# Performance work log

Measured on AMD Instinct MI355X. Metric: run time of the kernel, lower is better.

The kernel has to match this reference:

```python
import jax, jax.numpy as jnp
import numpy as np

LORA_DIM = 16          # hard-coded in module
LORA_TOKEN_INDEX = 1   # lora_dim*layer_sequence + 1 with layer_sequence=0
B, S, D, H = 4, 2048, 1024, 4096  # num_hiddens = 4*num_input (forced by view())


def setup_inputs() -> dict:
    key = jax.random.key(0)
    ks = jax.random.split(key, 6)
    x = jax.random.normal(ks[0], (B, S, D), dtype=jnp.float32)
    W1 = jax.random.normal(ks[1], (H, D), dtype=jnp.float32) * 0.02
    b1 = jnp.zeros((H,), dtype=jnp.float32)
    W2 = jax.random.normal(ks[2], (D, H), dtype=jnp.float32) * 0.02
    b2 = jnp.zeros((D,), dtype=jnp.float32)
    scale = jnp.asarray(0.001, dtype=jnp.float32)  # nn.Parameter(torch.tensor(0.001))
    return {"x": x, "W1": W1, "b1": b1, "W2": W2, "b2": b2, "scale": scale}


def reference(x, W1, b1, W2, b2, scale):
    Bx, Sx, Dx = x.shape
    Hx = W1.shape[0]  # = 4*Dx
    # 16 lora tokens starting at LORA_TOKEN_INDEX
    lt = jax.lax.dynamic_slice_in_dim(x, LORA_TOKEN_INDEX, LORA_DIM, axis=1)
    even = lt[:, ::2, :]  # (B, 8, D)
    odd = lt[:, 1::2, :]  # (B, 8, D)
    # per-sample low-rank weight updates:
    # result_multiplication[b,k] = outer(even[b,k], odd[b,k]) (D,D)
    # matrix1 = first 4 blocks stacked -> (B, 4D, D); matrix2 = last 4 reshaped -> (B, D, 4D)
    m1 = (even[:, :4, :, None] * odd[:, :4, None, :]).reshape(Bx, Hx, Dx)
    m2 = (even[:, 4:, :, None] * odd[:, 4:, None, :]).reshape(Bx, Dx, Hx)
    # x @ (W1 + scale*m1)^T + b1, fused without repeating W1 per batch
    h = jnp.einsum('bsd,hd->bsh', x, W1) + scale * jnp.einsum('bsd,bhd->bsh', x, m1) + b1
    h = jax.nn.gelu(h, approximate=False)  # torch nn.GELU default = exact erf
    out = jnp.einsum('bsh,oh->bso', h, W2) + scale * jnp.einsum('bsh,boh->bso', h, m2) + b2
    return out
```

## Files before the change

kernel.cpp:

```cpp
#include <hip/hip_runtime.h>
#include <cstdint>
#include <cstddef>

#define MROWS 8192
#define DDIM  1024
#define HDIM  4096

typedef __bf16 bf16x8 __attribute__((ext_vector_type(8)));
typedef float  f32x4  __attribute__((ext_vector_type(4)));

typedef __attribute__((address_space(1))) void* as1_vp;
typedef __attribute__((address_space(3))) void* as3_vp;

__device__ __forceinline__ unsigned short f2bf(float f) {
  unsigned int u = __builtin_bit_cast(unsigned int, f);
  u += 0x7fffu + ((u >> 16) & 1u);
  return (unsigned short)(u >> 16);
}
__device__ __forceinline__ float bf2f(unsigned short h) {
  return __builtin_bit_cast(float, (unsigned int)h << 16);
}

__device__ __forceinline__ float fast_gelu(float x) {
  float x3 = x * x * x;
  float z = 0.7978845608028654f * x + 0.03567740814f * x3;
  float e = __builtin_amdgcn_exp2f(z * 2.8853900817779268f);
  float t = 1.0f - 2.0f * __builtin_amdgcn_rcpf(e + 1.0f);
  return 0.5f * x * (1.0f + t);
}

__device__ __forceinline__ void gld_lds16(const unsigned short* g, unsigned short* lds) {
  __builtin_amdgcn_global_load_lds((as1_vp)(uintptr_t)g, (as3_vp)lds, 16, 0, 0);
}

__global__ __launch_bounds__(256) void pre_kernel(
    const float* __restrict__ x, const float* __restrict__ w1,
    const float* __restrict__ w2, unsigned short* __restrict__ xb,
    unsigned short* __restrict__ w1b, unsigned short* __restrict__ w2b,
    float* __restrict__ p1) {
  if (blockIdx.x < 8192) {
    int i = blockIdx.x * 256 + threadIdx.x;
    const float* src; unsigned short* dst; int off;
    if (i < 1048576) { src = w1; dst = w1b; off = i; }
    else             { src = w2; dst = w2b; off = i - 1048576; }
    float4 v = ((const float4*)src)[off];
    ushort4 o;
    o.x = f2bf(v.x); o.y = f2bf(v.y); o.z = f2bf(v.z); o.w = f2bf(v.w);
    ((ushort4*)dst)[off] = o;
    return;
  }
  const int bid = blockIdx.x - 8192;
  const int wave = threadIdx.x >> 6, lane = threadIdx.x & 63;
  const int m = bid * 4 + wave;
  const int b = m >> 11;
  const float4* xrow4 = (const float4*)(x + (size_t)m * DDIM);
  const float4* od4   = (const float4*)(x + ((size_t)b * 2048 + 2) * DDIM);
  ushort4* xbrow4 = (ushort4*)(xb + (size_t)m * DDIM);
  float a0 = 0.f, a1 = 0.f, a2 = 0.f, a3 = 0.f;
#pragma unroll
  for (int it = 0; it < 4; ++it) {
    int g = it * 64 + lane;
    float4 v = xrow4[g];
    ushort4 o; o.x = f2bf(v.x); o.y = f2bf(v.y); o.z = f2bf(v.z); o.w = f2bf(v.w);
    xbrow4[g] = o;
    float4 o0 = od4[g];
    float4 o1 = od4[512 + g];
    float4 o2 = od4[1024 + g];
    float4 o3 = od4[1536 + g];
    a0 += v.x * o0.x + v.y * o0.y + v.z * o0.z + v.w * o0.w;
    a1 += v.x * o1.x + v.y * o1.y + v.z * o1.z + v.w * o1.w;
    a2 += v.x * o2.x + v.y * o2.y + v.z * o2.z + v.w * o2.w;
    a3 += v.x * o3.x + v.y * o3.y + v.z * o3.z + v.w * o3.w;
  }
#pragma unroll
  for (int off = 32; off > 0; off >>= 1) {
    a0 += __shfl_down(a0, off);
    a1 += __shfl_down(a1, off);
    a2 += __shfl_down(a2, off);
    a3 += __shfl_down(a3, off);
  }
  if (lane == 0) {
    float4 r; r.x = a0; r.y = a1; r.z = a2; r.w = a3;
    ((float4*)p1)[m] = r;
  }
}

__global__ __launch_bounds__(256) void p2_kernel(const unsigned short* __restrict__ hact,
                                                 const float* __restrict__ x,
                                                 float* __restrict__ p2) {
  const int wave = threadIdx.x >> 6, lane = threadIdx.x & 63;
  const int m = blockIdx.x * 4 + wave;
  const int b = m >> 11;
  const ushort4* hrow4 = (const ushort4*)(hact + (size_t)m * HDIM);
  const float4* od4    = (const float4*)(x + ((size_t)b * 2048 + 10) * DDIM);
  float acc[4][4] = {{0.f}};
#pragma unroll
  for (int it = 0; it < 4; ++it) {
    int g = it * 64 + lane;
    float h[4][4];
#pragma unroll
    for (int r = 0; r < 4; ++r) {
      ushort4 hv = hrow4[r * 256 + g];
      h[r][0] = bf2f(hv.x); h[r][1] = bf2f(hv.y); h[r][2] = bf2f(hv.z); h[r][3] = bf2f(hv.w);
    }
#pragma unroll
    for (int i = 0; i < 4; ++i) {
      float4 ov = od4[i * 512 + g];
#pragma unroll
      for (int r = 0; r < 4; ++r)
        acc[i][r] += ov.x * h[r][0] + ov.y * h[r][1] + ov.z * h[r][2] + ov.w * h[r][3];
    }
  }
#pragma unroll
  for (int i = 0; i < 4; ++i)
#pragma unroll
    for (int r = 0; r < 4; ++r)
#pragma unroll
      for (int off = 32; off > 0; off >>= 1)
        acc[i][r] += __shfl_down(acc[i][r], off);
  if (lane == 0) {
#pragma unroll
    for (int i = 0; i < 4; ++i) {
      float4 v; v.x = acc[i][0]; v.y = acc[i][1]; v.z = acc[i][2]; v.w = acc[i][3];
      ((float4*)(p2 + (size_t)m * 16))[i] = v;
    }
  }
}

__device__ __forceinline__ void gemm_bt_tile64(const unsigned short* __restrict__ A,
                                               const unsigned short* __restrict__ B,
                                               const int ld, const int Kloop,
                                               const int m0, const int n0,
                                               unsigned short* As, unsigned short* Bs,
                                               f32x4 acc[4][4]) {
  const int tid  = threadIdx.x;
  const int wave = tid >> 6;
  const int lane = tid & 63;
  const int quad = lane >> 4;
  const int l16  = lane & 15;
  const int wm   = (wave >> 1) * 64;
  const int wn   = (wave & 1) * 64;

  const unsigned short* ga[4]; const unsigned short* gb[4];
#pragma unroll
  for (int s = 0; s < 4; ++s) {
    int idx = wave * 256 + s * 64 + lane;
    int r = idx >> 3, sl = idx & 7;
    int c = (sl - r) & 7;
    ga[s] = A + (size_t)(m0 + r) * ld + c * 8;
    gb[s] = B + (size_t)(n0 + r) * ld + c * 8;
  }

  for (int k0 = 0; k0 < Kloop; k0 += 64) {
    __syncthreads();
#pragma unroll
    for (int s = 0; s < 4; ++s) gld_lds16(ga[s] + k0, As + (wave * 4 + s) * 512);
#pragma unroll
    for (int s = 0; s < 4; ++s) gld_lds16(gb[s] + k0, Bs + (wave * 4 + s) * 512);
    __syncthreads();
#pragma unroll
    for (int kk = 0; kk < 64; kk += 32) {
      bf16x8 a[4], b[4];
      const int cbase = (kk >> 3) + quad;
#pragma unroll
      for (int i = 0; i < 4; ++i) {
        const int ra = wm + i * 16 + l16;
        const int rb = wn + i * 16 + l16;
        a[i] = *(const bf16x8*)(As + ra * 64 + ((cbase + ra) & 7) * 8);
        b[i] = *(const bf16x8*)(Bs + rb * 64 + ((cbase + rb) & 7) * 8);
      }
#pragma unroll
      for (int i = 0; i < 4; ++i)
#pragma unroll
        for (int j = 0; j < 4; ++j)
          acc[i][j] = __builtin_amdgcn_mfma_f32_16x16x32_bf16(a[i], b[j], acc[i][j], 0, 0, 0);
    }
  }
}

__global__ __launch_bounds__(256) void gemm1_kernel(
    const unsigned short* __restrict__ xb, const unsigned short* __restrict__ w1b,
    const float* __restrict__ x, const float* __restrict__ b1,
    const float* __restrict__ p1, const float* __restrict__ scale_p,
    unsigned short* __restrict__ hact) {
  __shared__ __align__(16) unsigned short As[128 * 64];
  __shared__ __align__(16) unsigned short Bs[128 * 64];
  const int id = blockIdx.x;
  const int xcd = id & 7, w = id >> 3;
  const int m0 = (xcd * 8 + (w & 7)) * 128;
  const int n0 = (w >> 3) * 128;
  f32x4 acc[4][4];
  const f32x4 z = {0.f, 0.f, 0.f, 0.f};
#pragma unroll
  for (int i = 0; i < 4; ++i)
#pragma unroll
    for (int j = 0; j < 4; ++j) acc[i][j] = z;

  gemm_bt_tile64(xb, w1b, DDIM, DDIM, m0, n0, As, Bs, acc);

  const int tid = threadIdx.x;
  const int wave = tid >> 6, lane = tid & 63, quad = lane >> 4, l16 = lane & 15;
  const int wm = (wave >> 1) * 64, wn = (wave & 1) * 64;
  const float sc = scale_p[0];
  const int bidx = m0 >> 11;
  const int i1 = (n0 + wn) >> 10;
  const float* exrow = x + ((size_t)(bidx * 2048 + 1 + 2 * i1)) * DDIM;

  float exv[4], b1v[4]; int nn[4];
#pragma unroll
  for (int j = 0; j < 4; ++j) {
    nn[j]  = n0 + wn + j * 16 + l16;
    exv[j] = exrow[nn[j] & 1023];
    b1v[j] = b1[nn[j]];
  }
#pragma unroll
  for (int i = 0; i < 4; ++i) {
#pragma unroll
    for (int r = 0; r < 4; ++r) {
      const int m = m0 + wm + i * 16 + quad * 4 + r;
      const float pv = p1[(size_t)m * 4 + i1] * sc;
#pragma unroll
      for (int j = 0; j < 4; ++j) {
        float v = acc[i][j][r] + b1v[j] + pv * exv[j];
        hact[(size_t)m * HDIM + nn[j]] = f2bf(fast_gelu(v));
      }
    }
  }
}

__global__ __launch_bounds__(256) void gemm2_kernel(
    const unsigned short* __restrict__ hact, const unsigned short* __restrict__ w2b,
    const float* __restrict__ x, const float* __restrict__ b2,
    const float* __restrict__ p2, const float* __restrict__ scale_p,
    float* __restrict__ out) {
  __shared__ __align__(16) unsigned short As[128 * 128];
  __shared__ __align__(16) unsigned short Bs[128 * 128];
  const int id = blockIdx.x;
  const int xcd = id & 7, w = id >> 3;
  const int m0 = (xcd * 8 + (w >> 3)) * 128;
  const int n0 = (w & 7) * 128;
  const int tid = threadIdx.x;
  const int wave = tid >> 6, lane = tid & 63, quad = lane >> 4, l16 = lane & 15;
  const int wm = (wave >> 1) * 64, wn = (wave & 1) * 64;
  f32x4 acc[4][4];
  const f32x4 z = {0.f, 0.f, 0.f, 0.f};
#pragma unroll
  for (int i = 0; i < 4; ++i)
#pragma unroll
    for (int j = 0; j < 4; ++j) acc[i][j] = z;

  const unsigned short* ga[8]; const unsigned short* gb[8];
#pragma unroll
  for (int s = 0; s < 8; ++s) {
    int idx = wave * 512 + s * 64 + lane;
    int r = idx >> 4, sl = idx & 15;
    int c = (sl - r) & 15;
    ga[s] = hact + (size_t)(m0 + r) * HDIM + c * 8;
    gb[s] = w2b  + (size_t)(n0 + r) * HDIM + c * 8;
  }

  for (int k0 = 0; k0 < HDIM; k0 += 128) {
    __syncthreads();
#pragma unroll
    for (int s = 0; s < 8; ++s) gld_lds16(ga[s] + k0, As + (wave * 8 + s) * 512);
#pragma unroll
    for (int s = 0; s < 8; ++s) gld_lds16(gb[s] + k0, Bs + (wave * 8 + s) * 512);
    __syncthreads();
#pragma unroll
    for (int kk = 0; kk < 128; kk += 32) {
      bf16x8 a[4], b[4];
      const int cbase = (kk >> 3) + quad;
#pragma unroll
      for (int i = 0; i < 4; ++i) {
        const int ra = wm + i * 16 + l16;
        const int rb = wn + i * 16 + l16;
        a[i] = *(const bf16x8*)(As + ra * 128 + ((cbase + ra) & 15) * 8);
        b[i] = *(const bf16x8*)(Bs + rb * 128 + ((cbase + rb) & 15) * 8);
      }
#pragma unroll
      for (int i = 0; i < 4; ++i)
#pragma unroll
        for (int j = 0; j < 4; ++j)
          acc[i][j] = __builtin_amdgcn_mfma_f32_16x16x32_bf16(a[i], b[j], acc[i][j], 0, 0, 0);
    }
  }

  const float sc = scale_p[0];
  const int bidx = m0 >> 11;
  const int i2 = (n0 + wn) >> 8;
  const float* evrow = x + ((size_t)(bidx * 2048 + 9 + 2 * i2)) * DDIM;

  float4 ev[4]; float b2v[4]; int nn[4];
#pragma unroll
  for (int j = 0; j < 4; ++j) {
    nn[j] = n0 + wn + j * 16 + l16;
    ev[j]  = *(const float4*)(evrow + 4 * (nn[j] & 255));
    b2v[j] = b2[nn[j]];
  }
#pragma unroll
  for (int i = 0; i < 4; ++i) {
#pragma unroll
    for (int r = 0; r < 4; ++r) {
      const int m = m0 + wm + i * 16 + quad * 4 + r;
      const float4 pv = *(const float4*)(p2 + (size_t)m * 16 + i2 * 4);
#pragma unroll
      for (int j = 0; j < 4; ++j) {
        float lora = ev[j].x * pv.x + ev[j].y * pv.y + ev[j].z * pv.z + ev[j].w * pv.w;
        out[(size_t)m * DDIM + nn[j]] = acc[i][j][r] + b2v[j] + sc * lora;
      }
    }
  }
}

extern "C" void kernel_launch(void* const* d_in, const int* in_sizes, int n_in,
                              void* d_out, int out_size, void* d_ws, size_t ws_size,
                              hipStream_t stream) {
  const float* x     = (const float*)d_in[0];
  const float* W1    = (const float*)d_in[1];
  const float* b1    = (const float*)d_in[2];
  const float* W2    = (const float*)d_in[3];
  const float* b2    = (const float*)d_in[4];
  const float* scale = (const float*)d_in[5];
  float* out = (float*)d_out;

  char* ws = (char*)d_ws;
  unsigned short* xb   = (unsigned short*)(ws);
  unsigned short* w1b  = (unsigned short*)(ws + 16777216);
  unsigned short* w2b  = (unsigned short*)(ws + 25165824);
  unsigned short* hact = (unsigned short*)(ws + 33554432);
  float*          p1   = (float*)(ws + 100663296);
  float*          p2   = (float*)(ws + 100794368);

  pre_kernel<<<dim3(10240), dim3(256), 0, stream>>>(x, W1, W2, xb, w1b, w2b, p1);
  gemm1_kernel<<<dim3(2048), dim3(256), 0, stream>>>(xb, w1b, x, b1, p1, scale, hact);
  p2_kernel<<<dim3(2048), dim3(256), 0, stream>>>(hact, x, p2);
  gemm2_kernel<<<dim3(512), dim3(256), 0, stream>>>(hact, w2b, x, b2, p2, scale, out);
}
```

Measured before the change: 282.9 us.

## Fuse p2 LoRA projection into gemm2 via extra MFMA on staged tiles

Removes the separate p2_kernel, which reread the whole bf16 hidden activation to project it onto the odd LoRA vectors. gemm2 now computes that projection inside its K loop: half the waves issue an extra MFMA per step against an odd-vector fragment kept in LDS (only lane column 0 nonzero), and write per-1024-segment partial sums to shared memory for the epilogue. This saves one full pass over hact and a kernel launch. In exchange it adds MFMA work and an imbalance between waves in gemm2, rounds the odd vector to bf16, and adds a little LDS.

```diff
diff --git a/kernel.cpp b/kernel.cpp
--- a/kernel.cpp
+++ b/kernel.cpp
@@ -85,48 +85,6 @@
   }
 }
 
-__global__ __launch_bounds__(256) void p2_kernel(const unsigned short* __restrict__ hact,
-                                                 const float* __restrict__ x,
-                                                 float* __restrict__ p2) {
-  const int wave = threadIdx.x >> 6, lane = threadIdx.x & 63;
-  const int m = blockIdx.x * 4 + wave;
-  const int b = m >> 11;
-  const ushort4* hrow4 = (const ushort4*)(hact + (size_t)m * HDIM);
-  const float4* od4    = (const float4*)(x + ((size_t)b * 2048 + 10) * DDIM);
-  float acc[4][4] = {{0.f}};
-#pragma unroll
-  for (int it = 0; it < 4; ++it) {
-    int g = it * 64 + lane;
-    float h[4][4];
-#pragma unroll
-    for (int r = 0; r < 4; ++r) {
-      ushort4 hv = hrow4[r * 256 + g];
-      h[r][0] = bf2f(hv.x); h[r][1] = bf2f(hv.y); h[r][2] = bf2f(hv.z); h[r][3] = bf2f(hv.w);
-    }
-#pragma unroll
-    for (int i = 0; i < 4; ++i) {
-      float4 ov = od4[i * 512 + g];
-#pragma unroll
-      for (int r = 0; r < 4; ++r)
-        acc[i][r] += ov.x * h[r][0] + ov.y * h[r][1] + ov.z * h[r][2] + ov.w * h[r][3];
-    }
-  }
-#pragma unroll
-  for (int i = 0; i < 4; ++i)
-#pragma unroll
-    for (int r = 0; r < 4; ++r)
-#pragma unroll
-      for (int off = 32; off > 0; off >>= 1)
-        acc[i][r] += __shfl_down(acc[i][r], off);
-  if (lane == 0) {
-#pragma unroll
-    for (int i = 0; i < 4; ++i) {
-      float4 v; v.x = acc[i][0]; v.y = acc[i][1]; v.z = acc[i][2]; v.w = acc[i][3];
-      ((float4*)(p2 + (size_t)m * 16))[i] = v;
-    }
-  }
-}
-
 __device__ __forceinline__ void gemm_bt_tile64(const unsigned short* __restrict__ A,
                                                const unsigned short* __restrict__ B,
                                                const int ld, const int Kloop,
@@ -231,10 +189,11 @@
 __global__ __launch_bounds__(256) void gemm2_kernel(
     const unsigned short* __restrict__ hact, const unsigned short* __restrict__ w2b,
     const float* __restrict__ x, const float* __restrict__ b2,
-    const float* __restrict__ p2, const float* __restrict__ scale_p,
-    float* __restrict__ out) {
+    const float* __restrict__ scale_p, float* __restrict__ out) {
   __shared__ __align__(16) unsigned short As[128 * 128];
   __shared__ __align__(16) unsigned short Bs[128 * 128];
+  __shared__ __align__(16) unsigned short od_lds[1024];
+  __shared__ __align__(16) float p2s[128 * 4];
   const int id = blockIdx.x;
   const int xcd = id & 7, w = id >> 3;
   const int m0 = (xcd * 8 + (w >> 3)) * 128;
@@ -242,12 +201,24 @@
   const int tid = threadIdx.x;
   const int wave = tid >> 6, lane = tid & 63, quad = lane >> 4, l16 = lane & 15;
   const int wm = (wave >> 1) * 64, wn = (wave & 1) * 64;
+  const int bidx = m0 >> 11;
+  const int i2 = n0 >> 8;
+
+  {
+    const float4* src = (const float4*)(x + ((size_t)(bidx * 2048 + 10 + 2 * i2)) * DDIM);
+    float4 v = src[tid];
+    ushort4 o; o.x = f2bf(v.x); o.y = f2bf(v.y); o.z = f2bf(v.z); o.w = f2bf(v.w);
+    ((ushort4*)od_lds)[tid] = o;
+  }
+
   f32x4 acc[4][4];
   const f32x4 z = {0.f, 0.f, 0.f, 0.f};
 #pragma unroll
   for (int i = 0; i < 4; ++i)
 #pragma unroll
     for (int j = 0; j < 4; ++j) acc[i][j] = z;
+  f32x4 pacc[4] = {z, z, z, z};
+  const bf16x8 zer8 = __builtin_bit_cast(bf16x8, z);
 
   const unsigned short* ga[8]; const unsigned short* gb[8];
 #pragma unroll
@@ -266,6 +237,7 @@
 #pragma unroll
     for (int s = 0; s < 8; ++s) gld_lds16(gb[s] + k0, Bs + (wave * 8 + s) * 512);
     __syncthreads();
+    const int odbase = k0 & 1023;
 #pragma unroll
     for (int kk = 0; kk < 128; kk += 32) {
       bf16x8 a[4], b[4];
@@ -277,17 +249,37 @@
         a[i] = *(const bf16x8*)(As + ra * 128 + ((cbase + ra) & 15) * 8);
         b[i] = *(const bf16x8*)(Bs + rb * 128 + ((cbase + rb) & 15) * 8);
       }
+      if (wn == 0) {
+        bf16x8 odv = *(const bf16x8*)(od_lds + odbase + kk + quad * 8);
+        bf16x8 bod = (l16 == 0) ? odv : zer8;
+#pragma unroll
+        for (int i = 0; i < 4; ++i)
+          pacc[i] = __builtin_amdgcn_mfma_f32_16x16x32_bf16(a[i], bod, pacc[i], 0, 0, 0);
+      }
 #pragma unroll
       for (int i = 0; i < 4; ++i)
 #pragma unroll
         for (int j = 0; j < 4; ++j)
           acc[i][j] = __builtin_amdgcn_mfma_f32_16x16x32_bf16(a[i], b[j], acc[i][j], 0, 0, 0);
     }
-  }
+    if (((k0 + 128) & 1023) == 0) {
+      const int seg = k0 >> 10;
+      if (wn == 0) {
+        if (l16 == 0) {
+#pragma unroll
+          for (int i = 0; i < 4; ++i)
+#pragma unroll
+            for (int e = 0; e < 4; ++e)
+              p2s[(wm + i * 16 + quad * 4 + e) * 4 + seg] = pacc[i][e];
+        }
+#pragma unroll
+        for (int i = 0; i < 4; ++i) pacc[i] = z;
+      }
+    }
+  }
+  __syncthreads();
 
   const float sc = scale_p[0];
-  const int bidx = m0 >> 11;
-  const int i2 = (n0 + wn) >> 8;
   const float* evrow = x + ((size_t)(bidx * 2048 + 9 + 2 * i2)) * DDIM;
 
   float4 ev[4]; float b2v[4]; int nn[4];
@@ -301,8 +293,9 @@
   for (int i = 0; i < 4; ++i) {
 #pragma unroll
     for (int r = 0; r < 4; ++r) {
-      const int m = m0 + wm + i * 16 + quad * 4 + r;
-      const float4 pv = *(const float4*)(p2 + (size_t)m * 16 + i2 * 4);
+      const int mloc = wm + i * 16 + quad * 4 + r;
+      const int m = m0 + mloc;
+      const float4 pv = *(const float4*)(p2s + mloc * 4);
 #pragma unroll
       for (int j = 0; j < 4; ++j) {
         float lora = ev[j].x * pv.x + ev[j].y * pv.y + ev[j].z * pv.z + ev[j].w * pv.w;
@@ -329,10 +322,8 @@
   unsigned short* w2b  = (unsigned short*)(ws + 25165824);
   unsigned short* hact = (unsigned short*)(ws + 33554432);
   float*          p1   = (float*)(ws + 100663296);
-  float*          p2   = (float*)(ws + 100794368);
 
   pre_kernel<<<dim3(10240), dim3(256), 0, stream>>>(x, W1, W2, xb, w1b, w2b, p1);
   gemm1_kernel<<<dim3(2048), dim3(256), 0, stream>>>(xb, w1b, x, b1, p1, scale, hact);
-  p2_kernel<<<dim3(2048), dim3(256), 0, stream>>>(hact, x, p2);
-  gemm2_kernel<<<dim3(512), dim3(256), 0, stream>>>(hact, w2b, x, b2, p2, scale, out);
-}
+  gemm2_kernel<<<dim3(512), dim3(256), 0, stream>>>(hact, w2b, x, b2, scale, out);
+}
```

Result: faster. 274.4 us (-3.0%).
